# Kernel optimization log

Measured on AMD Instinct MI355X. Metric: run time of the kernel, lower is better.

The kernel has to match this reference:

```python
import jax, jax.numpy as jnp
import numpy as np


def setup_inputs() -> dict:
    key = jax.random.key(0)
    k1, k2, k3 = jax.random.split(key, 3)
    B, S, H, D = 4, 4096, 16, 128
    C, K = H * D, 4
    return {
        "hidden_states": jax.random.normal(k1, (B, S, H, D), dtype=jnp.float32),
        "conv_weight": jax.random.normal(k2, (C, K), dtype=jnp.float32) * 0.1,
        "conv_bias": jax.random.normal(k3, (C,), dtype=jnp.float32) * 0.1,
    }


def reference(hidden_states, conv_weight, conv_bias):
    # hidden_states: [B, S, H, D] -> [B, C, S] with C = H*D
    B, S, H, D = hidden_states.shape
    C = H * D
    K = conv_weight.shape[-1]
    x = hidden_states.reshape(B, S, C).transpose(0, 2, 1)  # [B, C, S]
    # Depthwise causal conv1d: left-pad K-1, groups=C
    y = jax.lax.conv_general_dilated(
        x,
        conv_weight[:, None, :],  # [C, 1, K]
        window_strides=(1,),
        padding=[(K - 1, 0)],
        dimension_numbers=("NCH", "OIH", "NCH"),
        feature_group_count=C,
    )  # [B, C, S]
    y = jax.nn.silu(y + conv_bias[None, :, None])
    # reshape(bsz, n_heads, head_dim, seq_len).transpose(-1, -2)
    return y.reshape(B, H, D, S).transpose(0, 1, 3, 2)  # [B, H, S, D]
```

## Files before the change

kernel.cpp:

```cpp
#include <hip/hip_runtime.h>


constexpr int Bb = 4, Ss = 4096, Hh = 16, Dd = 128, Cc = 2048, Kk = 4;
constexpr int SEQ  = 8;
constexpr int CPB  = 1024;
constexpr int ROWS = SEQ + 3;

union F4 {
    float4 v;
    float f[4];
};

__device__ __forceinline__ void gload_lds16(const float* g, float* l) {
    __builtin_amdgcn_global_load_lds(
        (const __attribute__((address_space(1))) void*)g,
        (__attribute__((address_space(3))) void*)l,
        16, 0, 0);
}

__global__ __launch_bounds__(256, 3) void titans_conv(
    const float* __restrict__ x,
    const float* __restrict__ w,
    const float* __restrict__ bias,
    float* __restrict__ out)
{
    __shared__ float lds[ROWS * CPB];

    const int t  = threadIdx.x;
    const int wv = t >> 6;
    const int ln = t & 63;
    const int cb = (int)blockIdx.z * CPB;
    const int c0 = cb + t * 4;
    const int s0 = (int)blockIdx.x * SEQ;
    const int b  = (int)blockIdx.y;

    const float* xsrc = x + (size_t)b * Ss * Cc + cb + wv * 256 + ln * 4;

    float wf[4][4], bv[4];
    {
        const float4* wp = (const float4*)(w + (size_t)c0 * Kk);
        F4 u0, u1, u2, u3, ub;
        u0.v = wp[0]; u1.v = wp[1]; u2.v = wp[2]; u3.v = wp[3];
        ub.v = *(const float4*)(bias + c0);
        #pragma unroll
        for (int k = 0; k < 4; ++k) {
            wf[0][k] = u0.f[k]; wf[1][k] = u1.f[k];
            wf[2][k] = u2.f[k]; wf[3][k] = u3.f[k];
        }
        #pragma unroll
        for (int j = 0; j < 4; ++j) bv[j] = ub.f[j];
    }

    if (s0 >= 3) {
        #pragma unroll
        for (int r = 0; r < ROWS; ++r)
            gload_lds16(xsrc + (size_t)(s0 - 3 + r) * Cc,
                        &lds[r * CPB + wv * 256]);
    } else {
        #pragma unroll
        for (int r = 0; r < 3; ++r)
            *(float4*)&lds[r * CPB + t * 4] = float4{0.f, 0.f, 0.f, 0.f};
        #pragma unroll
        for (int r = 3; r < ROWS; ++r)
            gload_lds16(xsrc + (size_t)(s0 - 3 + r) * Cc,
                        &lds[r * CPB + wv * 256]);
    }

    __syncthreads();

    F4 rows[ROWS];
    #pragma unroll
    for (int r = 0; r < ROWS; ++r)
        rows[r].v = *(const float4*)&lds[r * CPB + t * 4];

    const int h = c0 >> 7;
    const int d = c0 & 127;
    float* orow = out + (((size_t)b * Hh + h) * Ss + s0) * Dd + d;

    #pragma unroll
    for (int i = 0; i < SEQ; ++i) {
        F4 res;
        #pragma unroll
        for (int j = 0; j < 4; ++j) {
            float z = bv[j];
            z = fmaf(wf[j][0], rows[i + 0].f[j], z);
            z = fmaf(wf[j][1], rows[i + 1].f[j], z);
            z = fmaf(wf[j][2], rows[i + 2].f[j], z);
            z = fmaf(wf[j][3], rows[i + 3].f[j], z);
            float e = __expf(-z);
            res.f[j] = z * __builtin_amdgcn_rcpf(1.0f + e);
        }
        *(float4*)(orow + (size_t)i * Dd) = res.v;
    }
}

extern "C" void kernel_launch(void* const* d_in, const int* in_sizes, int n_in,
                              void* d_out, int out_size, void* d_ws, size_t ws_size,
                              hipStream_t stream) {
    const float* x    = (const float*)d_in[0];
    const float* w    = (const float*)d_in[1];
    const float* bias = (const float*)d_in[2];
    float* out        = (float*)d_out;

    dim3 grid(Ss / SEQ, Bb, Cc / CPB);
    titans_conv<<<grid, 256, 0, stream>>>(x, w, bias, out);
}
```

Measured before the change: 232.8 us.

## Process 64-row sequence strips per block with a ring-buffered LDS prefetch

```diff
diff --git a/kernel.cpp b/kernel.cpp
--- a/kernel.cpp
+++ b/kernel.cpp
@@ -4,37 +4,40 @@
 constexpr int Bb = 4, Ss = 4096, Hh = 16, Dd = 128, Cc = 2048, Kk = 4;
 constexpr int SEQ  = 8;
 constexpr int CPB  = 1024;
-constexpr int ROWS = SEQ + 3;
+constexpr int TPB  = 8;
+constexpr int RING = 20;
+constexpr int STRIPS = Ss / (SEQ * TPB);
 
 union F4 {
     float4 v;
     float f[4];
 };
 
-__device__ __forceinline__ void gload_lds16(const float* g, float* l) {
+__device__ __forceinline__ void gload1k(const float* g, float* l) {
     __builtin_amdgcn_global_load_lds(
         (const __attribute__((address_space(1))) void*)g,
         (__attribute__((address_space(3))) void*)l,
         16, 0, 0);
 }
 
-__global__ __launch_bounds__(256, 3) void titans_conv(
+__global__ __launch_bounds__(256, 2) void titans_conv(
     const float* __restrict__ x,
     const float* __restrict__ w,
     const float* __restrict__ bias,
     float* __restrict__ out)
 {
-    __shared__ float lds[ROWS * CPB];
+    __shared__ float lds[RING * CPB];
 
-    const int t  = threadIdx.x;
-    const int wv = t >> 6;
-    const int ln = t & 63;
-    const int cb = (int)blockIdx.z * CPB;
-    const int c0 = cb + t * 4;
-    const int s0 = (int)blockIdx.x * SEQ;
-    const int b  = (int)blockIdx.y;
+    const int t     = threadIdx.x;
+    const int wv    = t >> 6;
+    const int ln    = t & 63;
+    const int strip = (int)blockIdx.x;
+    const int b     = (int)blockIdx.y;
+    const int cb    = (int)blockIdx.z * CPB;
+    const int c0    = cb + t * 4;
+    const int S0    = strip * (SEQ * TPB);
 
-    const float* xsrc = x + (size_t)b * Ss * Cc + cb + wv * 256 + ln * 4;
+    const float* xb = x + (size_t)b * Ss * Cc + cb;
 
     float wf[4][4], bv[4];
     {
@@ -51,46 +54,70 @@
         for (int j = 0; j < 4; ++j) bv[j] = ub.f[j];
     }
 
-    if (s0 >= 3) {
+    if (strip > 0) {
         #pragma unroll
-        for (int r = 0; r < ROWS; ++r)
-            gload_lds16(xsrc + (size_t)(s0 - 3 + r) * Cc,
-                        &lds[r * CPB + wv * 256]);
+        for (int k = 0; k < 11; ++k) {
+            const int sidx = wv * 11 + k;
+            const int lr = sidx >> 2, q = sidx & 3;
+            gload1k(xb + (size_t)(S0 - 3 + lr) * Cc + q * 256 + ln * 4,
+                    &lds[lr * CPB + q * 256]);
+        }
     } else {
         #pragma unroll
         for (int r = 0; r < 3; ++r)
             *(float4*)&lds[r * CPB + t * 4] = float4{0.f, 0.f, 0.f, 0.f};
         #pragma unroll
-        for (int r = 3; r < ROWS; ++r)
-            gload_lds16(xsrc + (size_t)(s0 - 3 + r) * Cc,
-                        &lds[r * CPB + wv * 256]);
+        for (int k = 0; k < 8; ++k) {
+            const int sidx = wv * 8 + k;
+            const int lr = 3 + (sidx >> 2), q = sidx & 3;
+            gload1k(xb + (size_t)(S0 - 3 + lr) * Cc + q * 256 + ln * 4,
+                    &lds[lr * CPB + q * 256]);
+        }
     }
-
     __syncthreads();
-
-    F4 rows[ROWS];
-    #pragma unroll
-    for (int r = 0; r < ROWS; ++r)
-        rows[r].v = *(const float4*)&lds[r * CPB + t * 4];
 
     const int h = c0 >> 7;
     const int d = c0 & 127;
-    float* orow = out + (((size_t)b * Hh + h) * Ss + s0) * Dd + d;
+    float* orow = out + (((size_t)b * Hh + h) * Ss + S0) * Dd + d;
 
     #pragma unroll
-    for (int i = 0; i < SEQ; ++i) {
-        F4 res;
+    for (int tt = 0; tt < TPB; ++tt) {
+        if (tt + 1 < TPB) {
+            const int base = (8 * tt + 11) % RING;
+            #pragma unroll
+            for (int k = 0; k < 8; ++k) {
+                const int rr = wv * 2 + (k >> 2);
+                const int q  = k & 3;
+                int sl = base + rr;
+                if (sl >= RING) sl -= RING;
+                gload1k(xb + (size_t)(S0 + 8 + 8 * tt + rr) * Cc + q * 256 + ln * 4,
+                        &lds[sl * CPB + q * 256]);
+            }
+        }
+
+        F4 rows[SEQ + 3];
         #pragma unroll
-        for (int j = 0; j < 4; ++j) {
-            float z = bv[j];
-            z = fmaf(wf[j][0], rows[i + 0].f[j], z);
-            z = fmaf(wf[j][1], rows[i + 1].f[j], z);
-            z = fmaf(wf[j][2], rows[i + 2].f[j], z);
-            z = fmaf(wf[j][3], rows[i + 3].f[j], z);
-            float e = __expf(-z);
-            res.f[j] = z * __builtin_amdgcn_rcpf(1.0f + e);
+        for (int i = 0; i < SEQ + 3; ++i) {
+            const int sl = (8 * tt + i) % RING;
+            rows[i].v = *(const float4*)&lds[sl * CPB + t * 4];
         }
-        *(float4*)(orow + (size_t)i * Dd) = res.v;
+        #pragma unroll
+        for (int i = 0; i < SEQ; ++i) {
+            F4 res;
+            #pragma unroll
+            for (int j = 0; j < 4; ++j) {
+                float z = bv[j];
+                z = fmaf(wf[j][0], rows[i + 0].f[j], z);
+                z = fmaf(wf[j][1], rows[i + 1].f[j], z);
+                z = fmaf(wf[j][2], rows[i + 2].f[j], z);
+                z = fmaf(wf[j][3], rows[i + 3].f[j], z);
+                float e = __expf(-z);
+                res.f[j] = z * __builtin_amdgcn_rcpf(1.0f + e);
+            }
+            *(float4*)(orow + (size_t)(tt * SEQ + i) * Dd) = res.v;
+        }
+
+        __syncthreads();
     }
 }
 
@@ -102,6 +129,6 @@
     const float* bias = (const float*)d_in[2];
     float* out        = (float*)d_out;
 
-    dim3 grid(Ss / SEQ, Bb, Cc / CPB);
+    dim3 grid(STRIPS, Bb, Cc / CPB);
     titans_conv<<<grid, 256, 0, stream>>>(x, w, bias, out);
 }
```

Result: slower. 240.0 us (+3.1%).
